# Kernel optimization log

Measured on AMD Instinct MI355X. Metric: run time of the kernel, lower is better.

## Reference

```python
import jax, jax.numpy as jnp
import numpy as np
import math

B, H, S, D = 2, 16, 2048, 64

def setup_inputs() -> dict:
    key = jax.random.key(0)
    kq, kk, kv = jax.random.split(key, 3)
    Q = jax.random.normal(kq, (B, H, S, D), dtype=jnp.float32)
    K = jax.random.normal(kk, (B, H, S, D), dtype=jnp.float32)
    V = jax.random.normal(kv, (B, H, S, D), dtype=jnp.float32)
    causal_mask = jnp.tril(jnp.ones((S, S), dtype=bool))
    return {"Q": Q, "K": K, "V": V, "causal_mask": causal_mask}

def reference(Q, K, V, causal_mask):
    d_k = K.shape[-1]
    scores = jnp.einsum('bhqd,bhkd->bhqk', Q, K) / math.sqrt(d_k)
    scores = jnp.where(causal_mask, scores, -jnp.inf)
    probs = jax.nn.softmax(scores, axis=-1)
    return jnp.einsum('bhqk,bhkd->bhqd', probs, V)
```

## Files before the change

kernel.cpp:

```cpp
#include <hip/hip_runtime.h>
#include <math.h>


constexpr int kS   = 2048;
constexpr int kD   = 64;
constexpr int kBH  = 32;
constexpr int kPadP = 72;

typedef short short8 __attribute__((ext_vector_type(8)));
typedef float float4v __attribute__((ext_vector_type(4)));
typedef float float16v __attribute__((ext_vector_type(16)));
typedef unsigned int u32;
typedef unsigned short u16;

static __device__ inline u16 f2bf(float f) {
  union { float f; unsigned u; } v; v.f = f;
  unsigned r = v.u + 0x7FFF + ((v.u >> 16) & 1);
  return (u16)(r >> 16);
}

static __device__ inline short8 pack8(float4v a, float4v b) {
  short8 r;
  r[0] = (short)f2bf(a[0]); r[1] = (short)f2bf(a[1]);
  r[2] = (short)f2bf(a[2]); r[3] = (short)f2bf(a[3]);
  r[4] = (short)f2bf(b[0]); r[5] = (short)f2bf(b[1]);
  r[6] = (short)f2bf(b[2]); r[7] = (short)f2bf(b[3]);
  return r;
}

static __device__ inline void async_cp16(const void* g, void* l) {
  __builtin_amdgcn_global_load_lds(
      (const __attribute__((address_space(1))) u32*)g,
      (__attribute__((address_space(3))) u32*)l, 16, 0, 0);
}

__global__ __launch_bounds__(256)
void prep_kernel(const float* __restrict__ K, const float* __restrict__ V,
                 u16* __restrict__ Kb, u16* __restrict__ VT) {
  __shared__ u16 tile[64 * kPadP];
  const int tid = threadIdx.x;
  const int bh = blockIdx.y, st = blockIdx.x;
  const size_t ibase = (size_t)bh * kS * kD + (size_t)st * 64 * kD;
  const int r  = tid >> 2;
  const int c0 = (tid & 3) * 16;
  {
    const float* kp = K + ibase + (size_t)r * kD + c0;
    float4v a = *(const float4v*)(kp);
    float4v b = *(const float4v*)(kp + 4);
    float4v c = *(const float4v*)(kp + 8);
    float4v d = *(const float4v*)(kp + 12);
    u16* dst = Kb + ibase + (size_t)r * kD + c0;
    *(short8*)dst       = pack8(a, b);
    *(short8*)(dst + 8) = pack8(c, d);
  }
  {
    const float* vp = V + ibase + (size_t)r * kD + c0;
    float4v a = *(const float4v*)(vp);
    float4v b = *(const float4v*)(vp + 4);
    float4v c = *(const float4v*)(vp + 8);
    float4v d = *(const float4v*)(vp + 12);
    u16* t = &tile[r * kPadP + c0];
    *(short8*)t       = pack8(a, b);
    *(short8*)(t + 8) = pack8(c, d);
  }
  __syncthreads();
  {
    const int dd = tid >> 2;
    const int s0 = (tid & 3) * 16;
    short8 w0, w1;
    #pragma unroll
    for (int i = 0; i < 8; ++i) {
      w0[i] = (short)tile[(s0 + i) * kPadP + dd];
      w1[i] = (short)tile[(s0 + 8 + i) * kPadP + dd];
    }
    u16* vdst = VT + (size_t)bh * kD * kS + (size_t)dd * kS + st * 64 + s0;
    *(short8*)vdst       = w0;
    *(short8*)(vdst + 8) = w1;
  }
}

__global__ __launch_bounds__(256, 4)
void fattn_kernel(const float* __restrict__ Q, const u16* __restrict__ Kb,
                  const u16* __restrict__ VT,
                  float* __restrict__ O0, float* __restrict__ O1,
                  float* __restrict__ O2, float* __restrict__ O3,
                  float* __restrict__ Lp) {
  __shared__ __align__(16) u16 ldsK[2][4096];
  __shared__ __align__(16) u16 ldsV[2][4096];

  const int tid  = threadIdx.x;
  const int wave = tid >> 6;
  const int lane = tid & 63;
  const int l31  = lane & 31;
  const int h    = lane >> 5;

  const int bh = blockIdx.y;
  const int p  = blockIdx.x >> 2;
  const int z  = blockIdx.x & 3;
  const int qiA = p, qiB = 15 - p;
  const int nA  = 2 * qiA + 2;

  const size_t base  = (size_t)bh * kS * kD;
  const size_t vbase = (size_t)bh * kD * kS;

  const int lr  = lane >> 3;
  const int cxl = (lane & 7) ^ lr;
  const int offK0 = lr * 64   + cxl * 8;
  const int offV0 = lr * 2048 + cxl * 8;
  const unsigned hs16 = ((unsigned)(h ^ (l31 & 7))) * 16;

  float* Od = (z == 0) ? O0 : (z == 1) ? O1 : (z == 2) ? O2 : O3;

  const int cB = (34 * z) / 4;
  const int cE = (34 * (z + 1)) / 4;

  int par = 0;
  for (int seg = 0; seg < 2; ++seg) {
    const int qi = seg ? qiB : qiA;
    int tb, te;
    if (seg == 0) { tb = min(cB, nA); te = min(cE, nA); }
    else          { tb = max(cB, nA) - nA; te = max(cE, nA) - nA; }
    const int q0  = qi * 128;
    const int wq0 = q0 + wave * 32;

    short8 qf[4];
    {
      const float scl = 0.125f * 1.44269504089f;
      const float* qp = Q + base + (size_t)(wq0 + l31) * kD + h * 8;
      #pragma unroll
      for (int dk = 0; dk < 4; ++dk) {
        float4v a = *(const float4v*)(qp + dk * 16);
        float4v b = *(const float4v*)(qp + dk * 16 + 4);
        #pragma unroll
        for (int i = 0; i < 4; ++i) { a[i] *= scl; b[i] *= scl; }
        qf[dk] = pack8(a, b);
      }
    }

    float16v acc0, acc1;
    #pragma unroll
    for (int i = 0; i < 16; ++i) { acc0[i] = 0.f; acc1[i] = 0.f; }
    float lacc = 0.f;

    if (tb < te) {
      {
        const u16* kg0 = Kb + base + (size_t)tb * 4096;
        const u16* vg0 = VT + vbase + tb * 64;
        const int b = par & 1;
        #pragma unroll
        for (int j = 0; j < 2; ++j) {
          const int g = wave + 4 * j;
          async_cp16(kg0 + g * 512 + offK0,   &ldsK[b][g * 512]);
          async_cp16(vg0 + (size_t)g * 16384 + offV0, &ldsV[b][g * 512]);
        }
      }
      for (int t = tb; t < te; ++t, ++par) {
        __syncthreads();
        if (t + 1 < te) {
          const u16* kg0 = Kb + base + (size_t)(t + 1) * 4096;
          const u16* vg0 = VT + vbase + (t + 1) * 64;
          const int b = (par + 1) & 1;
          #pragma unroll
          for (int j = 0; j < 2; ++j) {
            const int g = wave + 4 * j;
            async_cp16(kg0 + g * 512 + offK0,   &ldsK[b][g * 512]);
            async_cp16(vg0 + (size_t)g * 16384 + offV0, &ldsV[b][g * 512]);
          }
        }
        const char* KB = (const char*)ldsK[par & 1];
        const char* VB = (const char*)ldsV[par & 1];
        #pragma unroll
        for (int kt32 = 0; kt32 < 2; ++kt32) {
          const int ktb = t * 64 + kt32 * 32;
          if (ktb > wq0 + 31) break;

          float16v s;
          #pragma unroll
          for (int i = 0; i < 16; ++i) s[i] = 0.f;
          const char* krow = KB + (kt32 * 32 + l31) * 128;
          #pragma unroll
          for (int dk = 0; dk < 4; ++dk) {
            short8 kf = *(const short8*)(krow + (((unsigned)(dk * 32)) ^ hs16));
            s = __builtin_amdgcn_mfma_f32_32x32x16_bf16(kf, qf[dk], s, 0, 0, 0);
          }

          if (ktb + 31 > wq0) {
            const int qg = wq0 + l31;
            #pragma unroll
            for (int r = 0; r < 16; ++r) {
              const int kg = ktb + (r & 3) + 8 * (r >> 2) + 4 * h;
              if (kg > qg) s[r] = -1e30f;
            }
          }

          u32 pk[8];
          #pragma unroll
          for (int g2 = 0; g2 < 4; ++g2) {
            float p0 = __builtin_amdgcn_exp2f(s[4 * g2 + 0]);
            float p1 = __builtin_amdgcn_exp2f(s[4 * g2 + 1]);
            float p2 = __builtin_amdgcn_exp2f(s[4 * g2 + 2]);
            float p3 = __builtin_amdgcn_exp2f(s[4 * g2 + 3]);
            lacc += (p0 + p1) + (p2 + p3);
            pk[2 * g2]     = (__float_as_uint(p0) >> 16) | (__float_as_uint(p1) & 0xFFFF0000u);
            pk[2 * g2 + 1] = (__float_as_uint(p2) >> 16) | (__float_as_uint(p3) & 0xFFFF0000u);
          }
          u32 ek[8];
          #pragma unroll
          for (int i = 0; i < 8; ++i) ek[i] = (u32)__shfl_xor((int)pk[i], 32);

          #pragma unroll
          for (int c = 0; c < 2; ++c) {
            const int ga = 4 * c, gb = 4 * c + 2;
            union { u32 u[4]; short8 s8; } pf;
            pf.u[0] = h ? ek[gb]     : pk[ga];
            pf.u[1] = h ? ek[gb + 1] : pk[ga + 1];
            pf.u[2] = h ? pk[gb]     : ek[ga];
            pf.u[3] = h ? pk[gb + 1] : ek[ga + 1];
            const unsigned coff = ((unsigned)((kt32 * 4 + 2 * c) * 16)) ^ hs16;
            short8 vf0 = *(const short8*)(VB + l31 * 128 + coff);
            short8 vf1 = *(const short8*)(VB + (32 + l31) * 128 + coff);
            acc0 = __builtin_amdgcn_mfma_f32_32x32x16_bf16(pf.s8, vf0, acc0, 0, 0, 0);
            acc1 = __builtin_amdgcn_mfma_f32_32x32x16_bf16(pf.s8, vf1, acc1, 0, 0, 0);
          }
        }
      }
    }

    lacc += __shfl_xor(lacc, 32);
    if (h == 0) Lp[(size_t)z * kBH * kS + (size_t)bh * kS + wq0 + l31] = lacc;
    #pragma unroll
    for (int r = 0; r < 16; ++r) {
      const int row = (r & 3) + 8 * (r >> 2) + 4 * h;
      float* op = Od + base + (size_t)(wq0 + row) * kD + l31;
      op[0]  = acc0[r];
      op[32] = acc1[r];
    }
  }
}

__global__ __launch_bounds__(256)
void combine_kernel(const float* __restrict__ O1, const float* __restrict__ O2,
                    const float* __restrict__ O3, const float* __restrict__ Lp,
                    float* __restrict__ O) {
  const int idx4 = blockIdx.x * 256 + threadIdx.x;
  const int row  = idx4 >> 4;
  const int N = kBH * kS;
  const float l = Lp[row] + Lp[N + row] + Lp[2 * N + row] + Lp[3 * N + row];
  const float inv = 1.f / l;
  float4v a = ((const float4v*)O)[idx4];
  float4v b = ((const float4v*)O1)[idx4];
  float4v c = ((const float4v*)O2)[idx4];
  float4v d = ((const float4v*)O3)[idx4];
  #pragma unroll
  for (int i = 0; i < 4; ++i) a[i] = ((a[i] + b[i]) + (c[i] + d[i])) * inv;
  ((float4v*)O)[idx4] = a;
}

extern "C" void kernel_launch(void* const* d_in, const int* in_sizes, int n_in,
                              void* d_out, int out_size, void* d_ws, size_t ws_size,
                              hipStream_t stream) {
  const float* Q = (const float*)d_in[0];
  const float* K = (const float*)d_in[1];
  const float* V = (const float*)d_in[2];
  float* O = (float*)d_out;

  const size_t nKV = (size_t)kBH * kS * kD;
  u16* Kb = (u16*)d_ws;
  u16* VT = Kb + nKV;
  float* O1 = (float*)(VT + nKV);
  float* O2 = O1 + nKV;
  float* O3 = O2 + nKV;
  float* Lp = O3 + nKV;

  dim3 gprep(kS / 64, kBH);
  prep_kernel<<<gprep, 256, 0, stream>>>(K, V, Kb, VT);
  dim3 grid(32, kBH);
  fattn_kernel<<<grid, 256, 0, stream>>>(Q, Kb, VT, O, O1, O2, O3, Lp);
  combine_kernel<<<(int)(nKV / 4 / 256), 256, 0, stream>>>(O1, O2, O3, Lp, O);
}
```

Measured before the change: 147.4 us.

## Double per-wave query rows, store bf16 partials, compute row sums via MFMA

Each wave now handles 64 query rows (two 32-row groups), so every K and V fragment read from LDS is used twice. The grid halves to 16 blocks per head, and the occupancy hint drops to 2 blocks per CU. Q is scaled and converted to bf16 in the prep kernel. Partial outputs are stored as packed bf16 instead of fp32, which cuts split-K write and combine traffic at some cost in precision. Row sums come from an extra MFMA against a ones vector instead of scalar adds, and bf16 packing uses a perm instruction.

```diff
diff --git a/kernel.cpp b/kernel.cpp
--- a/kernel.cpp
+++ b/kernel.cpp
@@ -35,14 +35,28 @@
 }
 
 __global__ __launch_bounds__(256)
-void prep_kernel(const float* __restrict__ K, const float* __restrict__ V,
-                 u16* __restrict__ Kb, u16* __restrict__ VT) {
+void prep_kernel(const float* __restrict__ Q, const float* __restrict__ K,
+                 const float* __restrict__ V,
+                 u16* __restrict__ Qb, u16* __restrict__ Kb, u16* __restrict__ VT) {
   __shared__ u16 tile[64 * kPadP];
   const int tid = threadIdx.x;
   const int bh = blockIdx.y, st = blockIdx.x;
   const size_t ibase = (size_t)bh * kS * kD + (size_t)st * 64 * kD;
   const int r  = tid >> 2;
   const int c0 = (tid & 3) * 16;
+  {
+    const float scl = 0.125f * 1.44269504089f;
+    const float* qp = Q + ibase + (size_t)r * kD + c0;
+    float4v a = *(const float4v*)(qp);
+    float4v b = *(const float4v*)(qp + 4);
+    float4v c = *(const float4v*)(qp + 8);
+    float4v d = *(const float4v*)(qp + 12);
+    #pragma unroll
+    for (int i = 0; i < 4; ++i) { a[i] *= scl; b[i] *= scl; c[i] *= scl; d[i] *= scl; }
+    u16* dst = Qb + ibase + (size_t)r * kD + c0;
+    *(short8*)dst       = pack8(a, b);
+    *(short8*)(dst + 8) = pack8(c, d);
+  }
   {
     const float* kp = K + ibase + (size_t)r * kD + c0;
     float4v a = *(const float4v*)(kp);
@@ -79,11 +93,11 @@
   }
 }
 
-__global__ __launch_bounds__(256, 4)
-void fattn_kernel(const float* __restrict__ Q, const u16* __restrict__ Kb,
+__global__ __launch_bounds__(256, 2)
+void fattn_kernel(const u16* __restrict__ Qb, const u16* __restrict__ Kb,
                   const u16* __restrict__ VT,
-                  float* __restrict__ O0, float* __restrict__ O1,
-                  float* __restrict__ O2, float* __restrict__ O3,
+                  u32* __restrict__ O0, u32* __restrict__ O1,
+                  u32* __restrict__ O2, u32* __restrict__ O3,
                   float* __restrict__ Lp) {
   __shared__ __align__(16) u16 ldsK[2][4096];
   __shared__ __align__(16) u16 ldsV[2][4096];
@@ -97,8 +111,8 @@
   const int bh = blockIdx.y;
   const int p  = blockIdx.x >> 2;
   const int z  = blockIdx.x & 3;
-  const int qiA = p, qiB = 15 - p;
-  const int nA  = 2 * qiA + 2;
+  const int qiA = p, qiB = 7 - p;
+  const int nA  = 4 * p + 4;
 
   const size_t base  = (size_t)bh * kS * kD;
   const size_t vbase = (size_t)bh * kD * kS;
@@ -109,10 +123,13 @@
   const int offV0 = lr * 2048 + cxl * 8;
   const unsigned hs16 = ((unsigned)(h ^ (l31 & 7))) * 16;
 
-  float* Od = (z == 0) ? O0 : (z == 1) ? O1 : (z == 2) ? O2 : O3;
-
-  const int cB = (34 * z) / 4;
-  const int cE = (34 * (z + 1)) / 4;
+  u32* Od = (z == 0) ? O0 : (z == 1) ? O1 : (z == 2) ? O2 : O3;
+  const int cB = 9 * z;
+  const int cE = cB + 9;
+
+  short8 ones;
+  #pragma unroll
+  for (int i = 0; i < 8; ++i) ones[i] = (short)0x3F80;
 
   int par = 0;
   for (int seg = 0; seg < 2; ++seg) {
@@ -120,27 +137,22 @@
     int tb, te;
     if (seg == 0) { tb = min(cB, nA); te = min(cE, nA); }
     else          { tb = max(cB, nA) - nA; te = max(cE, nA) - nA; }
-    const int q0  = qi * 128;
-    const int wq0 = q0 + wave * 32;
-
-    short8 qf[4];
-    {
-      const float scl = 0.125f * 1.44269504089f;
-      const float* qp = Q + base + (size_t)(wq0 + l31) * kD + h * 8;
+    const int wq0 = qi * 256 + wave * 64;
+
+    short8 qf[2][4];
+    #pragma unroll
+    for (int g = 0; g < 2; ++g) {
+      const u16* qp = Qb + base + (size_t)(wq0 + 32 * g + l31) * kD + h * 8;
       #pragma unroll
-      for (int dk = 0; dk < 4; ++dk) {
-        float4v a = *(const float4v*)(qp + dk * 16);
-        float4v b = *(const float4v*)(qp + dk * 16 + 4);
-        #pragma unroll
-        for (int i = 0; i < 4; ++i) { a[i] *= scl; b[i] *= scl; }
-        qf[dk] = pack8(a, b);
-      }
-    }
-
-    float16v acc0, acc1;
-    #pragma unroll
-    for (int i = 0; i < 16; ++i) { acc0[i] = 0.f; acc1[i] = 0.f; }
-    float lacc = 0.f;
+      for (int dk = 0; dk < 4; ++dk) qf[g][dk] = *(const short8*)(qp + dk * 16);
+    }
+
+    float16v acc[2][2], lacc[2];
+    #pragma unroll
+    for (int g = 0; g < 2; ++g) {
+      #pragma unroll
+      for (int i = 0; i < 16; ++i) { acc[g][0][i] = 0.f; acc[g][1][i] = 0.f; lacc[g][i] = 0.f; }
+    }
 
     if (tb < te) {
       {
@@ -150,7 +162,7 @@
         #pragma unroll
         for (int j = 0; j < 2; ++j) {
           const int g = wave + 4 * j;
-          async_cp16(kg0 + g * 512 + offK0,   &ldsK[b][g * 512]);
+          async_cp16(kg0 + g * 512 + offK0,           &ldsK[b][g * 512]);
           async_cp16(vg0 + (size_t)g * 16384 + offV0, &ldsV[b][g * 512]);
         }
       }
@@ -163,7 +175,7 @@
           #pragma unroll
           for (int j = 0; j < 2; ++j) {
             const int g = wave + 4 * j;
-            async_cp16(kg0 + g * 512 + offK0,   &ldsK[b][g * 512]);
+            async_cp16(kg0 + g * 512 + offK0,           &ldsK[b][g * 512]);
             async_cp16(vg0 + (size_t)g * 16384 + offV0, &ldsV[b][g * 512]);
           }
         }
@@ -172,88 +184,109 @@
         #pragma unroll
         for (int kt32 = 0; kt32 < 2; ++kt32) {
           const int ktb = t * 64 + kt32 * 32;
-          if (ktb > wq0 + 31) break;
-
-          float16v s;
+          if (ktb > wq0 + 63) break;
+
+          const char* krow = KB + (kt32 * 32 + l31) * 128;
+          short8 kf[4];
           #pragma unroll
-          for (int i = 0; i < 16; ++i) s[i] = 0.f;
-          const char* krow = KB + (kt32 * 32 + l31) * 128;
-          #pragma unroll
-          for (int dk = 0; dk < 4; ++dk) {
-            short8 kf = *(const short8*)(krow + (((unsigned)(dk * 32)) ^ hs16));
-            s = __builtin_amdgcn_mfma_f32_32x32x16_bf16(kf, qf[dk], s, 0, 0, 0);
-          }
-
-          if (ktb + 31 > wq0) {
-            const int qg = wq0 + l31;
-            #pragma unroll
-            for (int r = 0; r < 16; ++r) {
-              const int kg = ktb + (r & 3) + 8 * (r >> 2) + 4 * h;
-              if (kg > qg) s[r] = -1e30f;
-            }
-          }
-
-          u32 pk[8];
-          #pragma unroll
-          for (int g2 = 0; g2 < 4; ++g2) {
-            float p0 = __builtin_amdgcn_exp2f(s[4 * g2 + 0]);
-            float p1 = __builtin_amdgcn_exp2f(s[4 * g2 + 1]);
-            float p2 = __builtin_amdgcn_exp2f(s[4 * g2 + 2]);
-            float p3 = __builtin_amdgcn_exp2f(s[4 * g2 + 3]);
-            lacc += (p0 + p1) + (p2 + p3);
-            pk[2 * g2]     = (__float_as_uint(p0) >> 16) | (__float_as_uint(p1) & 0xFFFF0000u);
-            pk[2 * g2 + 1] = (__float_as_uint(p2) >> 16) | (__float_as_uint(p3) & 0xFFFF0000u);
-          }
-          u32 ek[8];
-          #pragma unroll
-          for (int i = 0; i < 8; ++i) ek[i] = (u32)__shfl_xor((int)pk[i], 32);
-
+          for (int dk = 0; dk < 4; ++dk)
+            kf[dk] = *(const short8*)(krow + (((unsigned)(dk * 32)) ^ hs16));
+          short8 vf[4];
           #pragma unroll
           for (int c = 0; c < 2; ++c) {
-            const int ga = 4 * c, gb = 4 * c + 2;
-            union { u32 u[4]; short8 s8; } pf;
-            pf.u[0] = h ? ek[gb]     : pk[ga];
-            pf.u[1] = h ? ek[gb + 1] : pk[ga + 1];
-            pf.u[2] = h ? pk[gb]     : ek[ga];
-            pf.u[3] = h ? pk[gb + 1] : ek[ga + 1];
             const unsigned coff = ((unsigned)((kt32 * 4 + 2 * c) * 16)) ^ hs16;
-            short8 vf0 = *(const short8*)(VB + l31 * 128 + coff);
-            short8 vf1 = *(const short8*)(VB + (32 + l31) * 128 + coff);
-            acc0 = __builtin_amdgcn_mfma_f32_32x32x16_bf16(pf.s8, vf0, acc0, 0, 0, 0);
-            acc1 = __builtin_amdgcn_mfma_f32_32x32x16_bf16(pf.s8, vf1, acc1, 0, 0, 0);
+            vf[2 * c]     = *(const short8*)(VB + l31 * 128 + coff);
+            vf[2 * c + 1] = *(const short8*)(VB + (32 + l31) * 128 + coff);
+          }
+
+          #pragma unroll
+          for (int g = 0; g < 2; ++g) {
+            if (ktb > wq0 + 32 * g + 31) continue;
+
+            float16v s;
+            #pragma unroll
+            for (int i = 0; i < 16; ++i) s[i] = 0.f;
+            #pragma unroll
+            for (int dk = 0; dk < 4; ++dk)
+              s = __builtin_amdgcn_mfma_f32_32x32x16_bf16(kf[dk], qf[g][dk], s, 0, 0, 0);
+
+            if (ktb == wq0 + 32 * g) {
+              const int qg = wq0 + 32 * g + l31;
+              #pragma unroll
+              for (int r = 0; r < 16; ++r) {
+                const int kg = ktb + (r & 3) + 8 * (r >> 2) + 4 * h;
+                if (kg > qg) s[r] = -1e30f;
+              }
+            }
+
+            u32 pk[8];
+            #pragma unroll
+            for (int g2 = 0; g2 < 4; ++g2) {
+              const u32 u0 = __float_as_uint(__builtin_amdgcn_exp2f(s[4 * g2 + 0]));
+              const u32 u1 = __float_as_uint(__builtin_amdgcn_exp2f(s[4 * g2 + 1]));
+              const u32 u2 = __float_as_uint(__builtin_amdgcn_exp2f(s[4 * g2 + 2]));
+              const u32 u3 = __float_as_uint(__builtin_amdgcn_exp2f(s[4 * g2 + 3]));
+              pk[2 * g2]     = __builtin_amdgcn_perm(u1, u0, 0x07060302u);
+              pk[2 * g2 + 1] = __builtin_amdgcn_perm(u3, u2, 0x07060302u);
+            }
+            u32 ek[8];
+            #pragma unroll
+            for (int i = 0; i < 8; ++i) ek[i] = (u32)__shfl_xor((int)pk[i], 32);
+
+            #pragma unroll
+            for (int c = 0; c < 2; ++c) {
+              const int ga = 4 * c, gb = 4 * c + 2;
+              union { u32 u[4]; short8 s8; } pf;
+              pf.u[0] = h ? ek[gb]     : pk[ga];
+              pf.u[1] = h ? ek[gb + 1] : pk[ga + 1];
+              pf.u[2] = h ? pk[gb]     : ek[ga];
+              pf.u[3] = h ? pk[gb + 1] : ek[ga + 1];
+              acc[g][0] = __builtin_amdgcn_mfma_f32_32x32x16_bf16(pf.s8, vf[2 * c],     acc[g][0], 0, 0, 0);
+              acc[g][1] = __builtin_amdgcn_mfma_f32_32x32x16_bf16(pf.s8, vf[2 * c + 1], acc[g][1], 0, 0, 0);
+              lacc[g]   = __builtin_amdgcn_mfma_f32_32x32x16_bf16(pf.s8, ones,          lacc[g],   0, 0, 0);
+            }
           }
         }
       }
     }
 
-    lacc += __shfl_xor(lacc, 32);
-    if (h == 0) Lp[(size_t)z * kBH * kS + (size_t)bh * kS + wq0 + l31] = lacc;
-    #pragma unroll
-    for (int r = 0; r < 16; ++r) {
-      const int row = (r & 3) + 8 * (r >> 2) + 4 * h;
-      float* op = Od + base + (size_t)(wq0 + row) * kD + l31;
-      op[0]  = acc0[r];
-      op[32] = acc1[r];
+    #pragma unroll
+    for (int g = 0; g < 2; ++g) {
+      #pragma unroll
+      for (int r = 0; r < 16; ++r) {
+        const int row = (r & 3) + 8 * (r >> 2) + 4 * h;
+        const u32 w = (u32)f2bf(acc[g][0][r]) | ((u32)f2bf(acc[g][1][r]) << 16);
+        Od[((size_t)bh * kS + wq0 + 32 * g + row) * 32 + l31] = w;
+      }
+      if (l31 == 0) {
+        #pragma unroll
+        for (int r = 0; r < 16; ++r) {
+          const int row = (r & 3) + 8 * (r >> 2) + 4 * h;
+          Lp[(size_t)z * kBH * kS + (size_t)bh * kS + wq0 + 32 * g + row] = lacc[g][r];
+        }
+      }
     }
   }
 }
 
 __global__ __launch_bounds__(256)
-void combine_kernel(const float* __restrict__ O1, const float* __restrict__ O2,
-                    const float* __restrict__ O3, const float* __restrict__ Lp,
-                    float* __restrict__ O) {
-  const int idx4 = blockIdx.x * 256 + threadIdx.x;
-  const int row  = idx4 >> 4;
+void combine_kernel(const u32* __restrict__ O0, const u32* __restrict__ O1,
+                    const u32* __restrict__ O2, const u32* __restrict__ O3,
+                    const float* __restrict__ Lp, float* __restrict__ O) {
+  const int idx = blockIdx.x * 256 + threadIdx.x;
+  const int row = idx >> 5;
+  const int j   = idx & 31;
   const int N = kBH * kS;
   const float l = Lp[row] + Lp[N + row] + Lp[2 * N + row] + Lp[3 * N + row];
   const float inv = 1.f / l;
-  float4v a = ((const float4v*)O)[idx4];
-  float4v b = ((const float4v*)O1)[idx4];
-  float4v c = ((const float4v*)O2)[idx4];
-  float4v d = ((const float4v*)O3)[idx4];
-  #pragma unroll
-  for (int i = 0; i < 4; ++i) a[i] = ((a[i] + b[i]) + (c[i] + d[i])) * inv;
-  ((float4v*)O)[idx4] = a;
+  const u32 a = O0[idx], b = O1[idx], c = O2[idx], d = O3[idx];
+  const float lo = __uint_as_float(a << 16) + __uint_as_float(b << 16)
+                 + __uint_as_float(c << 16) + __uint_as_float(d << 16);
+  const float hi = __uint_as_float(a & 0xFFFF0000u) + __uint_as_float(b & 0xFFFF0000u)
+                 + __uint_as_float(c & 0xFFFF0000u) + __uint_as_float(d & 0xFFFF0000u);
+  float* op = O + (size_t)row * kD;
+  op[j]      = lo * inv;
+  op[j + 32] = hi * inv;
 }
 
 extern "C" void kernel_launch(void* const* d_in, const int* in_sizes, int n_in,
@@ -265,16 +298,18 @@
   float* O = (float*)d_out;
 
   const size_t nKV = (size_t)kBH * kS * kD;
-  u16* Kb = (u16*)d_ws;
+  u16* Qb = (u16*)d_ws;
+  u16* Kb = Qb + nKV;
   u16* VT = Kb + nKV;
-  float* O1 = (float*)(VT + nKV);
-  float* O2 = O1 + nKV;
-  float* O3 = O2 + nKV;
-  float* Lp = O3 + nKV;
+  u32* O0 = (u32*)(VT + nKV);
+  u32* O1 = O0 + nKV / 2;
+  u32* O2 = O1 + nKV / 2;
+  u32* O3 = O2 + nKV / 2;
+  float* Lp = (float*)(O3 + nKV / 2);
 
   dim3 gprep(kS / 64, kBH);
-  prep_kernel<<<gprep, 256, 0, stream>>>(K, V, Kb, VT);
-  dim3 grid(32, kBH);
-  fattn_kernel<<<grid, 256, 0, stream>>>(Q, Kb, VT, O, O1, O2, O3, Lp);
-  combine_kernel<<<(int)(nKV / 4 / 256), 256, 0, stream>>>(O1, O2, O3, Lp, O);
-}
+  prep_kernel<<<gprep, 256, 0, stream>>>(Q, K, V, Qb, Kb, VT);
+  dim3 grid(16, kBH);
+  fattn_kernel<<<grid, 256, 0, stream>>>(Qb, Kb, VT, O0, O1, O2, O3, Lp);
+  combine_kernel<<<(int)(kBH * kS * 32 / 256), 256, 0, stream>>>(O0, O1, O2, O3, Lp, O);
+}
```

After: 144.9 us. About the same (-1.7%).
